# Kernel optimization log

Measured on AMD Instinct MI355X. Metric: run time of the kernel, lower is better.

## Reference

```python
import jax, jax.numpy as jnp
import numpy as np

EMBED_DIM = 768
N_HEADS = 12
HEAD_SIZE = EMBED_DIM // N_HEADS
SCALE = HEAD_SIZE ** -0.5


def setup_inputs() -> dict:
    key = jax.random.key(0)
    k1, k2, k3, k4, k5 = jax.random.split(key, 5)
    B, T, C = 2, 4096, EMBED_DIM
    x = jax.random.normal(k1, (B, T, C), dtype=jnp.float32)
    # nn.Linear(embed_dim, 3*embed_dim): weight [3C, C], bias [3C]
    w_attn = jax.random.normal(k2, (3 * C, C), dtype=jnp.float32) * (C ** -0.5)
    b_attn = jax.random.normal(k3, (3 * C,), dtype=jnp.float32) * 0.02
    # nn.Linear(embed_dim, embed_dim)
    w_proj = jax.random.normal(k4, (C, C), dtype=jnp.float32) * (C ** -0.5)
    b_proj = jax.random.normal(k5, (C,), dtype=jnp.float32) * 0.02
    return {"x": x, "w_attn": w_attn, "b_attn": b_attn, "w_proj": w_proj, "b_proj": b_proj}


def reference(x, w_attn, b_attn, w_proj, b_proj):
    b, t, c = x.shape
    qkv = jnp.einsum('btc,dc->btd', x, w_attn) + b_attn  # [b,t,3c]
    q, k, v = jnp.split(qkv, 3, axis=-1)
    # [b, h, t, hs]
    q = q.reshape(b, t, N_HEADS, HEAD_SIZE).transpose(0, 2, 1, 3)
    k = k.reshape(b, t, N_HEADS, HEAD_SIZE).transpose(0, 2, 1, 3)
    v = v.reshape(b, t, N_HEADS, HEAD_SIZE).transpose(0, 2, 1, 3)
    scores = jnp.einsum('bhqd,bhkd->bhqk', q, k) * SCALE  # [b,h,t,t]
    causal = jnp.tril(jnp.ones((t, t), dtype=bool))
    scores = jnp.where(causal[None, None], scores, -jnp.inf)
    attn = jax.nn.softmax(scores, axis=-1)
    out = jnp.einsum('bhqk,bhkd->bhqd', attn, v)  # [b,h,t,hs]
    out = out.transpose(0, 2, 1, 3).reshape(b, t, c)
    out = jnp.einsum('btc,dc->btd', out, w_proj) + b_proj
    return out
```

## Files before the change

kernel.cpp:

```cpp
#include <hip/hip_runtime.h>
#include <hip/hip_bf16.h>

#define T_SEQ 4096
#define C_EMB 768
#define NH_ 12
#define HS_ 64
#define B_SZ 2
#define M_TOK 8192
#define N_QKV 2304

typedef __attribute__((ext_vector_type(8))) __bf16 bf16x8;
typedef __attribute__((ext_vector_type(8))) unsigned short ushort8v;
typedef __attribute__((ext_vector_type(2))) unsigned int uint2v;
typedef __attribute__((ext_vector_type(4))) unsigned int uint4v;
typedef __attribute__((ext_vector_type(4))) float f32x4;

__device__ __forceinline__ unsigned short f2bf(float f) {
  __hip_bfloat16 h = __float2bfloat16(f);
  return __builtin_bit_cast(unsigned short, h);
}

__device__ __forceinline__ unsigned int cvtpk(float lo, float hi) {
  unsigned int r;
  asm("v_cvt_pk_bf16_f32 %0, %1, %2" : "=v"(r) : "v"(lo), "v"(hi));
  return r;
}

#define KSWZ(row, bytecol) ((((row) * 128) + ((bytecol) ^ (((row) & 7) << 4))))

#define LOG2E 1.4426950408889634f

__global__ void cvt_f32_bf16(const float* __restrict__ in,
                             unsigned short* __restrict__ out) {
  int i = (blockIdx.x * 256 + threadIdx.x) * 8;
  float4 a = *reinterpret_cast<const float4*>(&in[i]);
  float4 b = *reinterpret_cast<const float4*>(&in[i + 4]);
  uint4v o;
  o.x = cvtpk(a.x, a.y);
  o.y = cvtpk(a.z, a.w);
  o.z = cvtpk(b.x, b.y);
  o.w = cvtpk(b.z, b.w);
  *reinterpret_cast<uint4v*>(&out[i]) = o;
}

template <int MODE>
__global__ __launch_bounds__(256) void gemm_bt_kernel(
    const unsigned short* __restrict__ A, const unsigned short* __restrict__ Bw,
    const float* __restrict__ bias, unsigned short* __restrict__ qo,
    unsigned short* __restrict__ ko, unsigned short* __restrict__ vo,
    float* __restrict__ fo, int Kdim, int Ndim) {
  __shared__ unsigned short as_[128 * 72];
  __shared__ unsigned short bs_[128 * 72];
  const int tid = threadIdx.x;
  const int lane = tid & 63;
  const int wid = tid >> 6;
  const int g = lane >> 4;
  const int l15 = lane & 15;
  const int m0 = blockIdx.y * 128;
  const int n0 = blockIdx.x * 128;
  const int wm = (wid >> 1) * 64;
  const int wn = (wid & 1) * 64;

  f32x4 acc[4][4];
#pragma unroll
  for (int i = 0; i < 4; ++i)
#pragma unroll
    for (int j = 0; j < 4; ++j) acc[i][j] = (f32x4){0.f, 0.f, 0.f, 0.f};

  for (int k0 = 0; k0 < Kdim; k0 += 64) {
#pragma unroll
    for (int it = 0; it < 4; ++it) {
      int cid = tid + it * 256;
      int r = cid >> 3, c8 = (cid & 7) << 3;
      *reinterpret_cast<ushort8v*>(&as_[r * 72 + c8]) =
          *reinterpret_cast<const ushort8v*>(&A[(size_t)(m0 + r) * Kdim + k0 + c8]);
      *reinterpret_cast<ushort8v*>(&bs_[r * 72 + c8]) =
          *reinterpret_cast<const ushort8v*>(&Bw[(size_t)(n0 + r) * Kdim + k0 + c8]);
    }
    __syncthreads();
#pragma unroll
    for (int ks = 0; ks < 2; ++ks) {
      bf16x8 af[4], bfr[4];
#pragma unroll
      for (int mf = 0; mf < 4; ++mf)
        af[mf] = __builtin_bit_cast(bf16x8,
            *reinterpret_cast<const ushort8v*>(&as_[(wm + mf * 16 + l15) * 72 + ks * 32 + g * 8]));
#pragma unroll
      for (int nf = 0; nf < 4; ++nf)
        bfr[nf] = __builtin_bit_cast(bf16x8,
            *reinterpret_cast<const ushort8v*>(&bs_[(wn + nf * 16 + l15) * 72 + ks * 32 + g * 8]));
#pragma unroll
      for (int mf = 0; mf < 4; ++mf)
#pragma unroll
        for (int nf = 0; nf < 4; ++nf)
          acc[mf][nf] = __builtin_amdgcn_mfma_f32_16x16x32_bf16(
              af[mf], bfr[nf], acc[mf][nf], 0, 0, 0);
    }
    __syncthreads();
  }

#pragma unroll
  for (int mf = 0; mf < 4; ++mf)
#pragma unroll
    for (int nf = 0; nf < 4; ++nf) {
      const int n = n0 + wn + nf * 16 + l15;
      const float bval = bias[n];
      float v4[4];
#pragma unroll
      for (int r2 = 0; r2 < 4; ++r2) v4[r2] = acc[mf][nf][r2] + bval;
      const int mb = m0 + wm + mf * 16 + g * 4;
      if (MODE == 1) {
#pragma unroll
        for (int r2 = 0; r2 < 4; ++r2)
          fo[(size_t)(mb + r2) * Ndim + n] = v4[r2];
      } else {
        const int which = (n >= 1536) ? 2 : ((n >= 768) ? 1 : 0);
        const int c = n - which * 768;
        const int h = c >> 6, d = c & 63;
        const int bI = mb >> 12, t = mb & 4095;
        if (which == 0) {
          const size_t off = ((size_t)(bI * NH_ + h) * T_SEQ + t) * HS_ + d;
#pragma unroll
          for (int r2 = 0; r2 < 4; ++r2)
            qo[off + (size_t)r2 * HS_] = f2bf(v4[r2] * 0.125f);
        } else if (which == 1) {
          const size_t off = ((size_t)(bI * NH_ + h) * T_SEQ + t) * HS_ + d;
#pragma unroll
          for (int r2 = 0; r2 < 4; ++r2)
            ko[off + (size_t)r2 * HS_] = f2bf(v4[r2]);
        } else {
          const size_t off = ((size_t)(bI * NH_ + h) * HS_ + d) * T_SEQ + t;
          uint2v o;
          o.x = cvtpk(v4[0], v4[1]);
          o.y = cvtpk(v4[2], v4[3]);
          *reinterpret_cast<uint2v*>(&vo[off]) = o;
        }
      }
    }
}

__global__ __launch_bounds__(256, 3) void flash_kernel(
    const unsigned short* __restrict__ Qg, const unsigned short* __restrict__ Kg,
    const unsigned short* __restrict__ Vtg, unsigned short* __restrict__ Og) {
  __shared__ __align__(16) char ksm[8192];
  __shared__ __align__(16) char vtm[8192];
  __shared__ __align__(16) char pls[16384];
  const int tid = threadIdx.x;
  const int lane = tid & 63;
  const int wid = tid >> 6;
  const int g = lane >> 4;
  const int l15 = lane & 15;

  const int cc = blockIdx.x & 255, kk = blockIdx.x >> 8;
  const int m = (kk == 0) ? (767 - cc) : ((kk == 1) ? (256 + cc) : cc);
  const int qt = m / 24;
  const int bh = m - qt * 24;
  const int q0 = qt * 128;
  const int b_ = bh / NH_, h_ = bh % NH_;
  const size_t kqbase = (size_t)bh * T_SEQ * HS_;
  const size_t vtbase = (size_t)bh * HS_ * T_SEQ;
  const int wq0 = wid * 32;

  bf16x8 qf[2][2];
#pragma unroll
  for (int nf = 0; nf < 2; ++nf)
#pragma unroll
    for (int ks = 0; ks < 2; ++ks)
      qf[nf][ks] = __builtin_bit_cast(bf16x8,
          *reinterpret_cast<const ushort8v*>(
              &Qg[kqbase + (size_t)(q0 + wq0 + nf * 16 + l15) * HS_ + ks * 32 + g * 8]));

  ushort8v ou;
#pragma unroll
  for (int j = 0; j < 8; ++j) ou[j] = 0x3f80;
  const bf16x8 ones_f = __builtin_bit_cast(bf16x8, ou);

  float m_run[2] = {-1e30f, -1e30f};
  float ml2[2] = {-1.4427e30f, -1.4427e30f};
  f32x4 oacc[2][4];
  f32x4 lacc[2];
#pragma unroll
  for (int nf = 0; nf < 2; ++nf) {
    lacc[nf] = (f32x4){0.f, 0.f, 0.f, 0.f};
#pragma unroll
    for (int j = 0; j < 4; ++j) oacc[nf][j] = (f32x4){0.f, 0.f, 0.f, 0.f};
  }

  char* pw = pls + wid * 4096;

  const int nkt = 2 * qt + 2;
  const int myt = ((q0 + wq0 + 31) >> 6) + 1;

  int sr[2], sc[2];
  const unsigned short* kgp[2];
  const unsigned short* vgp[2];
#pragma unroll
  for (int it = 0; it < 2; ++it) {
    int ci = tid + it * 256;
    sr[it] = ci >> 3;
    sc[it] = (ci & 7) * 16;
    kgp[it] = &Kg[kqbase + (size_t)sr[it] * HS_ + (sc[it] >> 1)];
    vgp[it] = &Vtg[vtbase + (size_t)sr[it] * T_SEQ + (sc[it] >> 1)];
  }

  ushort8v kreg[2], vreg[2];
#pragma unroll
  for (int it = 0; it < 2; ++it) {
    kreg[it] = *reinterpret_cast<const ushort8v*>(kgp[it]);
    vreg[it] = *reinterpret_cast<const ushort8v*>(vgp[it]);
  }

  for (int kt = 0; kt < nkt; ++kt) {
    __syncthreads();
#pragma unroll
    for (int it = 0; it < 2; ++it) {
      *reinterpret_cast<ushort8v*>(ksm + KSWZ(sr[it], sc[it])) = kreg[it];
      *reinterpret_cast<ushort8v*>(vtm + KSWZ(sr[it], sc[it])) = vreg[it];
    }
    if (kt + 1 < nkt) {
      const int k1 = (kt + 1) << 6;
#pragma unroll
      for (int it = 0; it < 2; ++it) {
        kreg[it] = *reinterpret_cast<const ushort8v*>(kgp[it] + (size_t)k1 * HS_);
        vreg[it] = *reinterpret_cast<const ushort8v*>(vgp[it] + k1);
      }
    }
    __syncthreads();

    if (kt < myt) {
      const int k0 = kt << 6;
      f32x4 st[4][2];
#pragma unroll
      for (int i = 0; i < 4; ++i)
#pragma unroll
        for (int j = 0; j < 2; ++j) st[i][j] = (f32x4){0.f, 0.f, 0.f, 0.f};
#pragma unroll
      for (int ks = 0; ks < 2; ++ks) {
        bf16x8 kf[4];
#pragma unroll
        for (int mf = 0; mf < 4; ++mf)
          kf[mf] = __builtin_bit_cast(bf16x8,
              *reinterpret_cast<const ushort8v*>(
                  ksm + KSWZ(mf * 16 + l15, ks * 64 + g * 16)));
#pragma unroll
        for (int mf = 0; mf < 4; ++mf)
#pragma unroll
          for (int nf = 0; nf < 2; ++nf)
            st[mf][nf] = __builtin_amdgcn_mfma_f32_16x16x32_bf16(
                kf[mf], qf[nf][ks], st[mf][nf], 0, 0, 0);
      }

      if (k0 + 63 > q0 + wq0) {
#pragma unroll
        for (int mf = 0; mf < 4; ++mf)
#pragma unroll
          for (int nf = 0; nf < 2; ++nf) {
            const int tq = q0 + wq0 + nf * 16 + l15;
#pragma unroll
            for (int r2 = 0; r2 < 4; ++r2) {
              const int tk = k0 + mf * 16 + g * 4 + r2;
              if (tk > tq) st[mf][nf][r2] = -1e30f;
            }
          }
      }

      float mx[2];
#pragma unroll
      for (int nf = 0; nf < 2; ++nf) {
        float v = fmaxf(fmaxf(st[0][nf][0], st[0][nf][1]),
                        fmaxf(st[0][nf][2], st[0][nf][3]));
        v = fmaxf(v, fmaxf(fmaxf(st[1][nf][0], st[1][nf][1]),
                           fmaxf(st[1][nf][2], st[1][nf][3])));
        v = fmaxf(v, fmaxf(fmaxf(st[2][nf][0], st[2][nf][1]),
                           fmaxf(st[2][nf][2], st[2][nf][3])));
        v = fmaxf(v, fmaxf(fmaxf(st[3][nf][0], st[3][nf][1]),
                           fmaxf(st[3][nf][2], st[3][nf][3])));
        v = fmaxf(v, __shfl_xor(v, 16));
        v = fmaxf(v, __shfl_xor(v, 32));
        mx[nf] = v;
      }
      if (__any((mx[0] > m_run[0] + 8.f) || (mx[1] > m_run[1] + 8.f))) {
#pragma unroll
        for (int nf = 0; nf < 2; ++nf) {
          const float mnew = fmaxf(m_run[nf], mx[nf]);
          const float alpha = exp2f((m_run[nf] - mnew) * LOG2E);
#pragma unroll
          for (int nd = 0; nd < 4; ++nd)
#pragma unroll
            for (int r2 = 0; r2 < 4; ++r2) oacc[nf][nd][r2] *= alpha;
#pragma unroll
          for (int r2 = 0; r2 < 4; ++r2) lacc[nf][r2] *= alpha;
          m_run[nf] = mnew;
          ml2[nf] = mnew * LOG2E;
        }
      }

#pragma unroll
      for (int mf = 0; mf < 4; ++mf)
#pragma unroll
        for (int nf = 0; nf < 2; ++nf) {
          const float p0 = exp2f(fmaf(st[mf][nf][0], LOG2E, -ml2[nf]));
          const float p1 = exp2f(fmaf(st[mf][nf][1], LOG2E, -ml2[nf]));
          const float p2 = exp2f(fmaf(st[mf][nf][2], LOG2E, -ml2[nf]));
          const float p3 = exp2f(fmaf(st[mf][nf][3], LOG2E, -ml2[nf]));
          uint2v w;
          w.x = cvtpk(p0, p1);
          w.y = cvtpk(p2, p3);
          *reinterpret_cast<uint2v*>(
              pw + KSWZ(nf * 16 + l15, mf * 32 + g * 8)) = w;
        }

#pragma unroll
      for (int ks = 0; ks < 2; ++ks) {
        bf16x8 pf[2];
#pragma unroll
        for (int nf = 0; nf < 2; ++nf)
          pf[nf] = __builtin_bit_cast(bf16x8,
              *reinterpret_cast<const ushort8v*>(
                  pw + KSWZ(nf * 16 + l15, ks * 64 + g * 16)));
        bf16x8 vt[4];
#pragma unroll
        for (int nd = 0; nd < 4; ++nd)
          vt[nd] = __builtin_bit_cast(bf16x8,
              *reinterpret_cast<const ushort8v*>(
                  vtm + KSWZ(nd * 16 + l15, ks * 64 + g * 16)));
#pragma unroll
        for (int nf = 0; nf < 2; ++nf) {
#pragma unroll
          for (int nd = 0; nd < 4; ++nd)
            oacc[nf][nd] = __builtin_amdgcn_mfma_f32_16x16x32_bf16(
                vt[nd], pf[nf], oacc[nf][nd], 0, 0, 0);
          lacc[nf] = __builtin_amdgcn_mfma_f32_16x16x32_bf16(
              ones_f, pf[nf], lacc[nf], 0, 0, 0);
        }
      }
    }
  }

#pragma unroll
  for (int nf = 0; nf < 2; ++nf) {
    const float invl = 1.f / lacc[nf][0];
    const int t = q0 + wq0 + nf * 16 + l15;
#pragma unroll
    for (int nd = 0; nd < 4; ++nd) {
      uint2v o;
      o.x = cvtpk(oacc[nf][nd][0] * invl, oacc[nf][nd][1] * invl);
      o.y = cvtpk(oacc[nf][nd][2] * invl, oacc[nf][nd][3] * invl);
      *reinterpret_cast<uint2v*>(
          &Og[((size_t)(b_ * T_SEQ + t)) * C_EMB + h_ * 64 + nd * 16 + g * 4]) = o;
    }
  }
}

extern "C" void kernel_launch(void* const* d_in, const int* in_sizes, int n_in,
                              void* d_out, int out_size, void* d_ws, size_t ws_size,
                              hipStream_t stream) {
  const float* x = (const float*)d_in[0];
  const float* w_attn = (const float*)d_in[1];
  const float* b_attn = (const float*)d_in[2];
  const float* w_proj = (const float*)d_in[3];
  const float* b_proj = (const float*)d_in[4];
  float* out = (float*)d_out;

  char* ws = (char*)d_ws;
  size_t off = 0;
  auto carve = [&](size_t bytes) -> void* {
    void* p = ws + off;
    off += (bytes + 255) & ~(size_t)255;
    return p;
  };
  unsigned short* xbf = (unsigned short*)carve((size_t)M_TOK * C_EMB * 2);
  unsigned short* wab = (unsigned short*)carve((size_t)N_QKV * C_EMB * 2);
  unsigned short* wpb = (unsigned short*)carve((size_t)C_EMB * C_EMB * 2);
  unsigned short* Qb = (unsigned short*)carve((size_t)B_SZ * NH_ * T_SEQ * HS_ * 2);
  unsigned short* Kb = (unsigned short*)carve((size_t)B_SZ * NH_ * T_SEQ * HS_ * 2);
  unsigned short* Vtb = (unsigned short*)carve((size_t)B_SZ * NH_ * T_SEQ * HS_ * 2);
  unsigned short* Ob = (unsigned short*)carve((size_t)M_TOK * C_EMB * 2);

  cvt_f32_bf16<<<3072, 256, 0, stream>>>(x, xbf);
  cvt_f32_bf16<<<864, 256, 0, stream>>>(w_attn, wab);
  cvt_f32_bf16<<<288, 256, 0, stream>>>(w_proj, wpb);

  gemm_bt_kernel<0><<<dim3(N_QKV / 128, M_TOK / 128), 256, 0, stream>>>(
      xbf, wab, b_attn, Qb, Kb, Vtb, nullptr, C_EMB, N_QKV);

  flash_kernel<<<dim3(768), 256, 0, stream>>>(Qb, Kb, Vtb, Ob);

  gemm_bt_kernel<1><<<dim3(C_EMB / 128, M_TOK / 128), 256, 0, stream>>>(
      Ob, wpb, b_proj, nullptr, nullptr, nullptr, out, C_EMB, C_EMB);
}
```

Before: 184.1 us.

## Double-buffer K/V shared tiles and use raw v_exp_f32 for softmax

Shared memory for the K and V^T tiles is now double-buffered. Each iteration writes the next tile into the alternate buffer while computing on the current one, which removes one __syncthreads per key tile, and global prefetch runs two tiles ahead. The exp2f calls are also replaced with inline v_exp_f32 asm, skipping the compiler's range-handling wrapper. Together this raises LDS use per block by 16 KB, which may hurt the occupancy target of 3 blocks, and drops exp2f's denormal and range handling.

```diff
diff --git a/kernel.cpp b/kernel.cpp
--- a/kernel.cpp
+++ b/kernel.cpp
@@ -23,6 +23,12 @@
 __device__ __forceinline__ unsigned int cvtpk(float lo, float hi) {
   unsigned int r;
   asm("v_cvt_pk_bf16_f32 %0, %1, %2" : "=v"(r) : "v"(lo), "v"(hi));
+  return r;
+}
+
+__device__ __forceinline__ float fast_exp2(float x) {
+  float r;
+  asm("v_exp_f32 %0, %1" : "=v"(r) : "v"(x));
   return r;
 }
 
@@ -142,8 +148,8 @@
 __global__ __launch_bounds__(256, 3) void flash_kernel(
     const unsigned short* __restrict__ Qg, const unsigned short* __restrict__ Kg,
     const unsigned short* __restrict__ Vtg, unsigned short* __restrict__ Og) {
-  __shared__ __align__(16) char ksm[8192];
-  __shared__ __align__(16) char vtm[8192];
+  __shared__ __align__(16) char ksm[2][8192];
+  __shared__ __align__(16) char vtm[2][8192];
   __shared__ __align__(16) char pls[16384];
   const int tid = threadIdx.x;
   const int lane = tid & 63;
@@ -209,26 +215,43 @@
     kreg[it] = *reinterpret_cast<const ushort8v*>(kgp[it]);
     vreg[it] = *reinterpret_cast<const ushort8v*>(vgp[it]);
   }
+#pragma unroll
+  for (int it = 0; it < 2; ++it) {
+    *reinterpret_cast<ushort8v*>(&ksm[0][KSWZ(sr[it], sc[it])]) = kreg[it];
+    *reinterpret_cast<ushort8v*>(&vtm[0][KSWZ(sr[it], sc[it])]) = vreg[it];
+  }
+  if (nkt > 1) {
+#pragma unroll
+    for (int it = 0; it < 2; ++it) {
+      kreg[it] = *reinterpret_cast<const ushort8v*>(kgp[it] + (size_t)64 * HS_);
+      vreg[it] = *reinterpret_cast<const ushort8v*>(vgp[it] + 64);
+    }
+  }
 
   for (int kt = 0; kt < nkt; ++kt) {
     __syncthreads();
-#pragma unroll
-    for (int it = 0; it < 2; ++it) {
-      *reinterpret_cast<ushort8v*>(ksm + KSWZ(sr[it], sc[it])) = kreg[it];
-      *reinterpret_cast<ushort8v*>(vtm + KSWZ(sr[it], sc[it])) = vreg[it];
-    }
+    const int cur = kt & 1;
     if (kt + 1 < nkt) {
-      const int k1 = (kt + 1) << 6;
 #pragma unroll
       for (int it = 0; it < 2; ++it) {
-        kreg[it] = *reinterpret_cast<const ushort8v*>(kgp[it] + (size_t)k1 * HS_);
-        vreg[it] = *reinterpret_cast<const ushort8v*>(vgp[it] + k1);
-      }
-    }
-    __syncthreads();
+        *reinterpret_cast<ushort8v*>(&ksm[cur ^ 1][KSWZ(sr[it], sc[it])]) = kreg[it];
+        *reinterpret_cast<ushort8v*>(&vtm[cur ^ 1][KSWZ(sr[it], sc[it])]) = vreg[it];
+      }
+      if (kt + 2 < nkt) {
+        const int k2 = (kt + 2) << 6;
+#pragma unroll
+        for (int it = 0; it < 2; ++it) {
+          kreg[it] = *reinterpret_cast<const ushort8v*>(kgp[it] + (size_t)k2 * HS_);
+          vreg[it] = *reinterpret_cast<const ushort8v*>(vgp[it] + k2);
+        }
+      }
+    }
 
     if (kt < myt) {
       const int k0 = kt << 6;
+      const char* kb = ksm[cur];
+      const char* vb = vtm[cur];
+
       f32x4 st[4][2];
 #pragma unroll
       for (int i = 0; i < 4; ++i)
@@ -241,7 +264,7 @@
         for (int mf = 0; mf < 4; ++mf)
           kf[mf] = __builtin_bit_cast(bf16x8,
               *reinterpret_cast<const ushort8v*>(
-                  ksm + KSWZ(mf * 16 + l15, ks * 64 + g * 16)));
+                  kb + KSWZ(mf * 16 + l15, ks * 64 + g * 16)));
 #pragma unroll
         for (int mf = 0; mf < 4; ++mf)
 #pragma unroll
@@ -283,7 +306,7 @@
 #pragma unroll
         for (int nf = 0; nf < 2; ++nf) {
           const float mnew = fmaxf(m_run[nf], mx[nf]);
-          const float alpha = exp2f((m_run[nf] - mnew) * LOG2E);
+          const float alpha = fast_exp2((m_run[nf] - mnew) * LOG2E);
 #pragma unroll
           for (int nd = 0; nd < 4; ++nd)
 #pragma unroll
@@ -299,10 +322,10 @@
       for (int mf = 0; mf < 4; ++mf)
 #pragma unroll
         for (int nf = 0; nf < 2; ++nf) {
-          const float p0 = exp2f(fmaf(st[mf][nf][0], LOG2E, -ml2[nf]));
-          const float p1 = exp2f(fmaf(st[mf][nf][1], LOG2E, -ml2[nf]));
-          const float p2 = exp2f(fmaf(st[mf][nf][2], LOG2E, -ml2[nf]));
-          const float p3 = exp2f(fmaf(st[mf][nf][3], LOG2E, -ml2[nf]));
+          const float p0 = fast_exp2(fmaf(st[mf][nf][0], LOG2E, -ml2[nf]));
+          const float p1 = fast_exp2(fmaf(st[mf][nf][1], LOG2E, -ml2[nf]));
+          const float p2 = fast_exp2(fmaf(st[mf][nf][2], LOG2E, -ml2[nf]));
+          const float p3 = fast_exp2(fmaf(st[mf][nf][3], LOG2E, -ml2[nf]));
           uint2v w;
           w.x = cvtpk(p0, p1);
           w.y = cvtpk(p2, p3);
@@ -323,7 +346,7 @@
         for (int nd = 0; nd < 4; ++nd)
           vt[nd] = __builtin_bit_cast(bf16x8,
               *reinterpret_cast<const ushort8v*>(
-                  vtm + KSWZ(nd * 16 + l15, ks * 64 + g * 16)));
+                  vb + KSWZ(nd * 16 + l15, ks * 64 + g * 16)));
 #pragma unroll
         for (int nf = 0; nf < 2; ++nf) {
 #pragma unroll
```

Measured after the change: 169.3 us. 1.09x faster.
